# Kernel optimization log

Measured on AMD Instinct MI355X. Metric: run time of the kernel, lower is better.

## Reference

```python
import jax, jax.numpy as jnp
import numpy as np

DENSITY = 0.1  # fraction of nonzero weights kept by the mask


def setup_inputs() -> dict:
    key = jax.random.key(0)
    k_data, k_w, k_m, k_b = jax.random.split(key, 4)
    M, N, K = 8192, 4096, 4096  # tokens, out_features, in_features
    data = jax.random.normal(k_data, (M, K), dtype=jnp.float32)
    weight = jax.random.normal(k_w, (N, K), dtype=jnp.float32)
    mask = (jax.random.uniform(k_m, (N, K)) < DENSITY).astype(jnp.float32)
    bias = jax.random.normal(k_b, (N,), dtype=jnp.float32)
    return {"data": data, "weight": weight, "mask": mask, "bias": bias}


def reference(data, weight, mask, bias):
    # Equivalent to cuSPARSE CSR SpMM with W_sparse = mask * weight, plus bias:
    # out = data @ (mask * weight)^T + bias  (same math as ref_forward / F.linear)
    w = mask * weight  # [N, K]
    out = jnp.einsum('mk,nk->mn', data, w) + bias  # [M, N]
    return out
```

## Files before the change

kernel.cpp:

```cpp
#include <hip/hip_runtime.h>
#include <hip/hip_bf16.h>


#define Mdim 8192
#define Ndim 4096
#define Kdim 4096

typedef __bf16 bf16x8 __attribute__((ext_vector_type(8)));
typedef float f32x4 __attribute__((ext_vector_type(4)));

__device__ inline unsigned short f2bf(float f) {
    union { float f; unsigned u; } v;
    v.f = f;
    unsigned r = v.u + 0x7fffu + ((v.u >> 16) & 1u);
    return (unsigned short)(r >> 16);
}

__device__ inline unsigned pack2(float a, float b) {
    return (unsigned)f2bf(a) | ((unsigned)f2bf(b) << 16);
}

#define GLOAD_LDS16(gp, lp)                                                     \
    __builtin_amdgcn_global_load_lds((const __attribute__((address_space(1))) void*)(gp), \
                                     (__attribute__((address_space(3))) void*)(lp), 16, 0, 0)

#define VMCNT_I(n)  asm volatile("s_waitcnt vmcnt(" #n ")" ::: "memory")
#define VMCNT(n)    VMCNT_I(n)
#define FENCE()     asm volatile("" ::: "memory")
#define BARRIER()   do { FENCE(); __builtin_amdgcn_s_barrier(); FENCE(); } while (0)

__global__ __launch_bounds__(256) void k_cvt_all(const float4* __restrict__ data,
                                                 const float4* __restrict__ weight,
                                                 const float4* __restrict__ mask,
                                                 uint4* __restrict__ Abf,
                                                 uint4* __restrict__ Bbf) {
    const int NA = Mdim * (Kdim / 8);
    const int NB = Ndim * (Kdim / 8);
    const int stride = gridDim.x * blockDim.x;
    for (int i = blockIdx.x * blockDim.x + threadIdx.x; i < NA + NB; i += stride) {
        if (i < NA) {
            const size_t j2 = 2 * (size_t)i;
            float4 v0 = data[j2], v1 = data[j2 + 1];
            uint4 o;
            o.x = pack2(v0.x, v0.y); o.y = pack2(v0.z, v0.w);
            o.z = pack2(v1.x, v1.y); o.w = pack2(v1.z, v1.w);
            Abf[i] = o;
        } else {
            const size_t j = (size_t)(i - NA);
            const size_t j2 = 2 * j;
            float4 w0 = weight[j2], w1 = weight[j2 + 1];
            float4 m0 = mask[j2],   m1 = mask[j2 + 1];
            uint4 o;
            o.x = pack2(w0.x * m0.x, w0.y * m0.y);
            o.y = pack2(w0.z * m0.z, w0.w * m0.w);
            o.z = pack2(w1.x * m1.x, w1.y * m1.y);
            o.w = pack2(w1.z * m1.z, w1.w * m1.w);
            Bbf[j] = o;
        }
    }
}

__global__ __launch_bounds__(512, 2) void k_gemm256(const unsigned short* __restrict__ A,
                                                    const unsigned short* __restrict__ B,
                                                    const float* __restrict__ bias,
                                                    float* __restrict__ out) {
    __shared__ __align__(16) unsigned short sh[4 * 16384];

    const int tid  = threadIdx.x;
    const int lane = tid & 63;
    const int wave = tid >> 6;

    const int bid = blockIdx.x;
    const int swz = (bid & 7) * 64 + (bid >> 3);
    const int bm  = (swz & 31) * 256;
    const int bn  = (swz >> 5) * 256;

    const int rrow = lane >> 3;
    const int scol = ((lane & 7) ^ rrow) * 8;
    const int ldsl = lane * 8;
    const int w8   = wave * 8;
    const int rbB  = (wave >> 2) * 64 + (wave & 3) * 8;

    const int dstA0 = w8 * 64 + ldsl;
    const int dstA1 = (64 + w8) * 64 + ldsl;
    const int dstB0 = 8192 + w8 * 64 + ldsl;
    const int dstB1 = 8192 + (64 + w8) * 64 + ldsl;

    const int fr = lane & 15;
    const int kc = lane >> 4;
    const int po = (kc ^ (fr & 7)) * 8;
    const int arow = ((wave >> 2) * 64 + fr) * 64;
    const int brow = ((wave & 3) * 32 + fr) * 64;

    const unsigned short* pA0 = A + (size_t)(bm + w8 + rrow) * Kdim + scol;
    const unsigned short* pA1 = pA0 + (size_t)128 * Kdim;
    const unsigned short* pA2 = pA0 + (size_t)64 * Kdim;
    const unsigned short* pA3 = pA0 + (size_t)192 * Kdim;
    const unsigned short* pB0 = B + (size_t)(bn + rbB + rrow) * Kdim + scol;
    const unsigned short* pB1 = pB0 + (size_t)128 * Kdim;
    const unsigned short* pB2 = pB0 + (size_t)32 * Kdim;
    const unsigned short* pB3 = pB0 + (size_t)160 * Kdim;

    f32x4 acc[8][4];
#pragma unroll
    for (int i = 0; i < 8; ++i)
#pragma unroll
        for (int j = 0; j < 4; ++j) acc[i][j] = (f32x4){0.f, 0.f, 0.f, 0.f};

    bf16x8 a0[4][2], a1[4][2], b0[2][2], b1[2][2];

#define READ_A4(dst, base) do {                                                  \
    _Pragma("unroll")                                                            \
    for (int _i = 0; _i < 4; ++_i) {                                             \
        dst[_i][0] = *(const bf16x8*)&sh[(base) + _i * 1024 + po];               \
        dst[_i][1] = *(const bf16x8*)&sh[(base) + _i * 1024 + (po ^ 32)];        \
    } } while (0)

#define READ_B2(dst, base) do {                                                  \
    _Pragma("unroll")                                                            \
    for (int _j = 0; _j < 2; ++_j) {                                             \
        dst[_j][0] = *(const bf16x8*)&sh[(base) + _j * 1024 + po];               \
        dst[_j][1] = *(const bf16x8*)&sh[(base) + _j * 1024 + (po ^ 32)];        \
    } } while (0)

#define Q_MFMA(AF, BF, IO, JO) do {                                              \
    __builtin_amdgcn_s_setprio(1);                                               \
    _Pragma("unroll")                                                            \
    for (int _i = 0; _i < 4; ++_i) {                                             \
        _Pragma("unroll")                                                        \
        for (int _j = 0; _j < 2; ++_j) {                                         \
            acc[(IO)+_i][(JO)+_j] = __builtin_amdgcn_mfma_f32_16x16x32_bf16(     \
                AF[_i][0], BF[_j][0], acc[(IO)+_i][(JO)+_j], 0, 0, 0);           \
            acc[(IO)+_i][(JO)+_j] = __builtin_amdgcn_mfma_f32_16x16x32_bf16(     \
                AF[_i][1], BF[_j][1], acc[(IO)+_i][(JO)+_j], 0, 0, 0);           \
        } }                                                                      \
    __builtin_amdgcn_s_setprio(0); } while (0)

#define KTILE(W0_, W1_, W2_, DOSTAGE, DOTAIL, EB, OB, EB2) do {                  \
                                                     \
    VMCNT(W0_); BARRIER();                                                       \
    Q_MFMA(a0, b0, 0, 0);                                                        \
                                                     \
    READ_A4(a1, (OB) + arow);                                                    \
    VMCNT(W1_); BARRIER();                                                       \
    if (DOSTAGE) {                                                               \
        GLOAD_LDS16(pA0, sh + (EB) + dstA0);                                     \
        GLOAD_LDS16(pA1, sh + (EB) + dstA1);                                     \
        GLOAD_LDS16(pB0, sh + (EB) + dstB0);                                     \
        GLOAD_LDS16(pB1, sh + (EB) + dstB1);                                     \
    }                                                                            \
    Q_MFMA(a1, b0, 4, 0);                                                        \
                                                     \
    READ_B2(b1, (OB) + 8192 + brow);                                             \
    VMCNT(W2_); BARRIER();                                                       \
    if (DOSTAGE) {                                                               \
        GLOAD_LDS16(pA2, sh + (OB) + dstA0);                                     \
        GLOAD_LDS16(pA3, sh + (OB) + dstA1);                                     \
    }                                                                            \
    Q_MFMA(a1, b1, 4, 2);                                                        \
                                                     \
    BARRIER();                                                                   \
    if (DOSTAGE) {                                                               \
        GLOAD_LDS16(pB2, sh + (OB) + dstB0);                                     \
        GLOAD_LDS16(pB3, sh + (OB) + dstB1);                                     \
        pA0 += 64; pA1 += 64; pA2 += 64; pA3 += 64;                              \
        pB0 += 64; pB1 += 64; pB2 += 64; pB3 += 64;                              \
    }                                                                            \
    Q_MFMA(a0, b1, 0, 2);                                                        \
    if (DOTAIL) {        \
        READ_A4(a0, (EB2) + arow);                                               \
        READ_B2(b0, (EB2) + 8192 + brow);                                        \
    } } while (0)

    GLOAD_LDS16(pA0, sh + 0 + dstA0);      GLOAD_LDS16(pA1, sh + 0 + dstA1);
    GLOAD_LDS16(pB0, sh + 0 + dstB0);      GLOAD_LDS16(pB1, sh + 0 + dstB1);
    GLOAD_LDS16(pA2, sh + 16384 + dstA0);  GLOAD_LDS16(pA3, sh + 16384 + dstA1);
    GLOAD_LDS16(pB2, sh + 16384 + dstB0);  GLOAD_LDS16(pB3, sh + 16384 + dstB1);
    GLOAD_LDS16(pA0 + 64, sh + 32768 + dstA0); GLOAD_LDS16(pA1 + 64, sh + 32768 + dstA1);
    GLOAD_LDS16(pB0 + 64, sh + 32768 + dstB0); GLOAD_LDS16(pB1 + 64, sh + 32768 + dstB1);
    GLOAD_LDS16(pA2 + 64, sh + 49152 + dstA0); GLOAD_LDS16(pA3 + 64, sh + 49152 + dstA1);
    GLOAD_LDS16(pB2 + 64, sh + 49152 + dstB0); GLOAD_LDS16(pB3 + 64, sh + 49152 + dstB1);
    pA0 += 128; pA1 += 128; pA2 += 128; pA3 += 128;
    pB0 += 128; pB1 += 128; pB2 += 128; pB3 += 128;

    VMCNT(12);
    BARRIER();
    READ_A4(a0, 0 + arow);
    READ_B2(b0, 0 + 8192 + brow);

    for (int t2 = 0; t2 < 31; ++t2) {
        KTILE(10, 8, 8, true, true, 0,     16384, 32768);
        KTILE(10, 8, 8, true, true, 32768, 49152, 0);
    }
    KTILE(10, 8, 4, false, true, 0, 16384, 32768);
    KTILE(2, 0, 0, false, false, 32768, 49152, 0);

    const int wm = (wave >> 2) * 128;
    const int wn = (wave & 3) * 64;
    const int colb = bn + wn + fr;
    const int rowb = bm + wm + (lane >> 4) * 4;
#pragma unroll
    for (int jg = 0; jg < 4; ++jg) {
        const int col = colb + jg * 16;
        const float bv = bias[col];
#pragma unroll
        for (int ig = 0; ig < 8; ++ig) {
            const int row = rowb + ig * 16;
            float* op = out + (size_t)row * Ndim + col;
#pragma unroll
            for (int r = 0; r < 4; ++r) op[(size_t)r * Ndim] = acc[ig][jg][r] + bv;
        }
    }
#undef KTILE
#undef Q_MFMA
#undef READ_A4
#undef READ_B2
}

__global__ void k_naive(const float* __restrict__ A, const float* __restrict__ W,
                        const float* __restrict__ Msk, const float* __restrict__ bias,
                        float* __restrict__ out) {
    int n = blockIdx.x * blockDim.x + threadIdx.x;
    int m = blockIdx.y;
    if (n >= Ndim) return;
    const float* a = A + (size_t)m * Kdim;
    const float* w = W + (size_t)n * Kdim;
    const float* mk = Msk + (size_t)n * Kdim;
    float s = 0.f;
    for (int k = 0; k < Kdim; ++k) s += a[k] * w[k] * mk[k];
    out[(size_t)m * Ndim + n] = s + bias[n];
}

extern "C" void kernel_launch(void* const* d_in, const int* in_sizes, int n_in,
                              void* d_out, int out_size, void* d_ws, size_t ws_size,
                              hipStream_t stream) {
    const float* data   = (const float*)d_in[0];
    const float* weight = (const float*)d_in[1];
    const float* mask   = (const float*)d_in[2];
    const float* bias   = (const float*)d_in[3];
    float* out = (float*)d_out;

    const size_t needA = (size_t)Mdim * Kdim * 2;
    const size_t needB = (size_t)Ndim * Kdim * 2;
    if (ws_size < needA + needB) {
        dim3 g((Ndim + 255) / 256, Mdim);
        k_naive<<<g, 256, 0, stream>>>(data, weight, mask, bias, out);
        return;
    }

    unsigned short* Abf = (unsigned short*)d_ws;
    unsigned short* Bbf = Abf + (size_t)Mdim * Kdim;

    k_cvt_all<<<4096, 256, 0, stream>>>((const float4*)data, (const float4*)weight,
                                        (const float4*)mask, (uint4*)Abf, (uint4*)Bbf);

    k_gemm256<<<dim3(512), dim3(512), 0, stream>>>(Abf, Bbf, bias, out);
}
```

Measured before the change: 591.7 us.

## Restructure GEMM main loop into double-buffered 256x64 stages with fine-grained barriers

Replaces the four-slot LDS ring holding half-tile stages with two full 256x64 K-slice buffers. Global-to-LDS staging is now split into quarter-chunks interleaved between MFMA groups, with a barrier around every MFMA quadrant. The staging layout moves from per-wave rows to per-thread contiguous rows. The aim is smoother overlap of loads with compute, at the cost of many more barriers per iteration.

```diff
diff --git a/kernel.cpp b/kernel.cpp
--- a/kernel.cpp
+++ b/kernel.cpp
@@ -24,10 +24,9 @@
     __builtin_amdgcn_global_load_lds((const __attribute__((address_space(1))) void*)(gp), \
                                      (__attribute__((address_space(3))) void*)(lp), 16, 0, 0)
 
-#define VMCNT_I(n)  asm volatile("s_waitcnt vmcnt(" #n ")" ::: "memory")
-#define VMCNT(n)    VMCNT_I(n)
-#define FENCE()     asm volatile("" ::: "memory")
-#define BARRIER()   do { FENCE(); __builtin_amdgcn_s_barrier(); FENCE(); } while (0)
+#define VMCNT(n)  asm volatile("s_waitcnt vmcnt(" #n ")" ::: "memory")
+#define FENCE()   asm volatile("" ::: "memory")
+#define BARRIER() do { FENCE(); __builtin_amdgcn_s_barrier(); FENCE(); } while (0)
 
 __global__ __launch_bounds__(256) void k_cvt_all(const float4* __restrict__ data,
                                                  const float4* __restrict__ weight,
@@ -64,7 +63,9 @@
                                                     const unsigned short* __restrict__ B,
                                                     const float* __restrict__ bias,
                                                     float* __restrict__ out) {
-    __shared__ __align__(16) unsigned short sh[4 * 16384];
+    __shared__ __align__(16) unsigned short sh[2 * 32768];
+#define DB0 0
+#define DB1 32768
 
     const int tid  = threadIdx.x;
     const int lane = tid & 63;
@@ -75,31 +76,22 @@
     const int bm  = (swz & 31) * 256;
     const int bn  = (swz >> 5) * 256;
 
-    const int rrow = lane >> 3;
-    const int scol = ((lane & 7) ^ rrow) * 8;
-    const int ldsl = lane * 8;
-    const int w8   = wave * 8;
-    const int rbB  = (wave >> 2) * 64 + (wave & 3) * 8;
-
-    const int dstA0 = w8 * 64 + ldsl;
-    const int dstA1 = (64 + w8) * 64 + ldsl;
-    const int dstB0 = 8192 + w8 * 64 + ldsl;
-    const int dstB1 = 8192 + (64 + w8) * 64 + ldsl;
+    const int srow = tid >> 3;
+    const int scol = ((tid & 7) ^ (srow & 7)) * 8;
+    const int sdst = tid * 8;
+    const unsigned short* pAg = A + (size_t)(bm + srow) * Kdim + scol;
+    const unsigned short* pBg = B + (size_t)(bn + srow) * Kdim + scol;
 
     const int fr = lane & 15;
     const int kc = lane >> 4;
     const int po = (kc ^ (fr & 7)) * 8;
-    const int arow = ((wave >> 2) * 64 + fr) * 64;
-    const int brow = ((wave & 3) * 32 + fr) * 64;
-
-    const unsigned short* pA0 = A + (size_t)(bm + w8 + rrow) * Kdim + scol;
-    const unsigned short* pA1 = pA0 + (size_t)128 * Kdim;
-    const unsigned short* pA2 = pA0 + (size_t)64 * Kdim;
-    const unsigned short* pA3 = pA0 + (size_t)192 * Kdim;
-    const unsigned short* pB0 = B + (size_t)(bn + rbB + rrow) * Kdim + scol;
-    const unsigned short* pB1 = pB0 + (size_t)128 * Kdim;
-    const unsigned short* pB2 = pB0 + (size_t)32 * Kdim;
-    const unsigned short* pB3 = pB0 + (size_t)160 * Kdim;
+    const int arow = ((wave >> 2) * 128 + fr) * 64;
+    const int brow = ((wave & 3) * 64 + fr) * 64;
+
+#define STG_A(db, k0, grow) GLOAD_LDS16(pAg + (size_t)(grow) * Kdim + (k0),      \
+                                        sh + (db) + (grow) * 64 + sdst)
+#define STG_B(db, k0, grow) GLOAD_LDS16(pBg + (size_t)(grow) * Kdim + (k0),      \
+                                        sh + (db) + 16384 + (grow) * 64 + sdst)
 
     f32x4 acc[8][4];
 #pragma unroll
@@ -136,64 +128,50 @@
         } }                                                                      \
     __builtin_amdgcn_s_setprio(0); } while (0)
 
-#define KTILE(W0_, W1_, W2_, DOSTAGE, DOTAIL, EB, OB, EB2) do {                  \
-                                                     \
-    VMCNT(W0_); BARRIER();                                                       \
-    Q_MFMA(a0, b0, 0, 0);                                                        \
-                                                     \
-    READ_A4(a1, (OB) + arow);                                                    \
-    VMCNT(W1_); BARRIER();                                                       \
-    if (DOSTAGE) {                                                               \
-        GLOAD_LDS16(pA0, sh + (EB) + dstA0);                                     \
-        GLOAD_LDS16(pA1, sh + (EB) + dstA1);                                     \
-        GLOAD_LDS16(pB0, sh + (EB) + dstB0);                                     \
-        GLOAD_LDS16(pB1, sh + (EB) + dstB1);                                     \
-    }                                                                            \
-    Q_MFMA(a1, b0, 4, 0);                                                        \
-                                                     \
-    READ_B2(b1, (OB) + 8192 + brow);                                             \
-    VMCNT(W2_); BARRIER();                                                       \
-    if (DOSTAGE) {                                                               \
-        GLOAD_LDS16(pA2, sh + (OB) + dstA0);                                     \
-        GLOAD_LDS16(pA3, sh + (OB) + dstA1);                                     \
-    }                                                                            \
-    Q_MFMA(a1, b1, 4, 2);                                                        \
-                                                     \
-    BARRIER();                                                                   \
-    if (DOSTAGE) {                                                               \
-        GLOAD_LDS16(pB2, sh + (OB) + dstB0);                                     \
-        GLOAD_LDS16(pB3, sh + (OB) + dstB1);                                     \
-        pA0 += 64; pA1 += 64; pA2 += 64; pA3 += 64;                              \
-        pB0 += 64; pB1 += 64; pB2 += 64; pB3 += 64;                              \
-    }                                                                            \
-    Q_MFMA(a0, b1, 0, 2);                                                        \
-    if (DOTAIL) {        \
-        READ_A4(a0, (EB2) + arow);                                               \
-        READ_B2(b0, (EB2) + 8192 + brow);                                        \
-    } } while (0)
-
-    GLOAD_LDS16(pA0, sh + 0 + dstA0);      GLOAD_LDS16(pA1, sh + 0 + dstA1);
-    GLOAD_LDS16(pB0, sh + 0 + dstB0);      GLOAD_LDS16(pB1, sh + 0 + dstB1);
-    GLOAD_LDS16(pA2, sh + 16384 + dstA0);  GLOAD_LDS16(pA3, sh + 16384 + dstA1);
-    GLOAD_LDS16(pB2, sh + 16384 + dstB0);  GLOAD_LDS16(pB3, sh + 16384 + dstB1);
-    GLOAD_LDS16(pA0 + 64, sh + 32768 + dstA0); GLOAD_LDS16(pA1 + 64, sh + 32768 + dstA1);
-    GLOAD_LDS16(pB0 + 64, sh + 32768 + dstB0); GLOAD_LDS16(pB1 + 64, sh + 32768 + dstB1);
-    GLOAD_LDS16(pA2 + 64, sh + 49152 + dstA0); GLOAD_LDS16(pA3 + 64, sh + 49152 + dstA1);
-    GLOAD_LDS16(pB2 + 64, sh + 49152 + dstB0); GLOAD_LDS16(pB3 + 64, sh + 49152 + dstB1);
-    pA0 += 128; pA1 += 128; pA2 += 128; pA3 += 128;
-    pB0 += 128; pB1 += 128; pB2 += 128; pB3 += 128;
-
-    VMCNT(12);
-    BARRIER();
-    READ_A4(a0, 0 + arow);
-    READ_B2(b0, 0 + 8192 + brow);
-
-    for (int t2 = 0; t2 < 31; ++t2) {
-        KTILE(10, 8, 8, true, true, 0,     16384, 32768);
-        KTILE(10, 8, 8, true, true, 32768, 49152, 0);
-    }
-    KTILE(10, 8, 4, false, true, 0, 16384, 32768);
-    KTILE(2, 0, 0, false, false, 32768, 49152, 0);
+#define ITER(kb, SB1, SA2, SB2, SA3, W4M) do {                                   \
+                                                                \
+    if (SB1) { STG_B(DB1, (kb)+64, 0);  STG_B(DB1, (kb)+64, 64); }               \
+    VMCNT(6); BARRIER();                                                         \
+    READ_A4(a0, DB0 + arow); READ_B2(b0, DB0 + 16384 + brow);                    \
+    Q_MFMA(a0, b0, 0, 0); BARRIER();                                             \
+                                                                \
+    READ_A4(a1, DB0 + 4096 + arow);                                              \
+    if (SB1) { STG_B(DB1, (kb)+64, 128); STG_B(DB1, (kb)+64, 192); }             \
+    BARRIER(); Q_MFMA(a1, b0, 4, 0); BARRIER();                                  \
+                                                                \
+    READ_B2(b1, DB0 + 16384 + 2048 + brow);                                      \
+    if (SA2) { STG_A(DB0, (kb)+128, 0);  STG_A(DB0, (kb)+128, 64); }             \
+    BARRIER(); Q_MFMA(a1, b1, 4, 2); BARRIER();                                  \
+                                                                \
+    if (SA2) { STG_A(DB0, (kb)+128, 128); STG_A(DB0, (kb)+128, 192); }           \
+    BARRIER(); Q_MFMA(a0, b1, 0, 2); BARRIER();                                  \
+                                                              \
+    if (SB2) { STG_B(DB0, (kb)+128, 0);  STG_B(DB0, (kb)+128, 64); }             \
+    W4M; BARRIER();                                                              \
+    READ_A4(a0, DB1 + arow); READ_B2(b0, DB1 + 16384 + brow);                    \
+    Q_MFMA(a0, b0, 0, 0); BARRIER();                                             \
+                                                              \
+    READ_A4(a1, DB1 + 4096 + arow);                                              \
+    if (SB2) { STG_B(DB0, (kb)+128, 128); STG_B(DB0, (kb)+128, 192); }           \
+    BARRIER(); Q_MFMA(a1, b0, 4, 0); BARRIER();                                  \
+                                                              \
+    READ_B2(b1, DB1 + 16384 + 2048 + brow);                                      \
+    if (SA3) { STG_A(DB1, (kb)+192, 0);  STG_A(DB1, (kb)+192, 64); }             \
+    BARRIER(); Q_MFMA(a1, b1, 4, 2); BARRIER();                                  \
+                                                              \
+    if (SA3) { STG_A(DB1, (kb)+192, 128); STG_A(DB1, (kb)+192, 192); }           \
+    BARRIER(); Q_MFMA(a0, b1, 0, 2); BARRIER();                                  \
+} while (0)
+
+    STG_A(DB0, 0, 0);  STG_A(DB0, 0, 64);  STG_A(DB0, 0, 128);  STG_A(DB0, 0, 192);
+    STG_B(DB0, 0, 0);  STG_B(DB0, 0, 64);  STG_B(DB0, 0, 128);  STG_B(DB0, 0, 192);
+    STG_A(DB1, 64, 0); STG_A(DB1, 64, 64); STG_A(DB1, 64, 128); STG_A(DB1, 64, 192);
+
+    for (int i = 0; i < 31; ++i) {
+        const int kb = i * 128;
+        ITER(kb, true, true, true, true, VMCNT(6));
+    }
+    ITER(3968, true, false, false, false, VMCNT(0));
 
     const int wm = (wave >> 2) * 128;
     const int wn = (wave & 3) * 64;
@@ -211,10 +189,14 @@
             for (int r = 0; r < 4; ++r) op[(size_t)r * Ndim] = acc[ig][jg][r] + bv;
         }
     }
-#undef KTILE
+#undef ITER
 #undef Q_MFMA
 #undef READ_A4
 #undef READ_B2
+#undef STG_A
+#undef STG_B
+#undef DB0
+#undef DB1
 }
 
 __global__ void k_naive(const float* __restrict__ A, const float* __restrict__ W,
```

Measured after the change: 540.9 us. 8.6% less time.
